# Optimization experiments

Hardware: AMD Instinct MI355X
Metric: run time of the kernel (lower is better)

## Reference

```python
import jax, jax.numpy as jnp
import numpy as np

BATCH = 2_000_000
IN_DIM = 10
OUT_DIM = 3


def setup_inputs() -> dict:
    key = jax.random.key(0)
    kx, kw, km = jax.random.split(key, 3)
    x = jax.random.normal(kx, (BATCH, IN_DIM), dtype=jnp.float32)
    W = jax.random.normal(kw, (OUT_DIM, IN_DIM), dtype=jnp.float32)
    # M initialized near identity (well-conditioned), matching torch.eye init
    M = jnp.eye(OUT_DIM, dtype=jnp.float32) + 0.1 * jax.random.normal(km, (OUT_DIM, OUT_DIM), dtype=jnp.float32)
    return {"x": x, "W": W, "M": M}


def reference(x, W, M):
    det_A = jnp.linalg.det(M)
    is_singular = jnp.isclose(det_A, jnp.float32(0.0))  # torch.isclose defaults: rtol=1e-5, atol=1e-8
    M_inv = jnp.linalg.inv(M)
    M_inv = jnp.where(is_singular, jnp.full_like(M_inv, jnp.nan), M_inv)
    # y = (M_inv @ W @ x.T).T == x @ (M_inv @ W).T
    proj = M_inv @ W                      # [out, in] tiny matmul
    return x @ proj.T                     # [batch, out]
```

## Files before the change

kernel.cpp:

```cpp
#include <hip/hip_runtime.h>

#define IN_DIM 10
#define OUT_DIM 3
#define BLOCK 256

__global__ __launch_bounds__(BLOCK, 6) void simnet_direct(
    const float* __restrict__ x,
    const float* __restrict__ W,
    const float* __restrict__ M,
    float* __restrict__ out,
    long long batch)
{
    const long long npairs = batch >> 1;
    const long long p = (long long)blockIdx.x * BLOCK + threadIdx.x;
    if (p >= npairs) return;

    const float4* xv = reinterpret_cast<const float4*>(x) + 5 * p;
    const float4 v0 = xv[0];
    const float4 v1 = xv[1];
    const float4 v2 = xv[2];
    const float4 v3 = xv[3];
    const float4 v4 = xv[4];

    const float a = M[0], b = M[1], c = M[2];
    const float d = M[3], e = M[4], f_ = M[5];
    const float g = M[6], h = M[7], i_ = M[8];
    const float A =  (e * i_ - f_ * h);
    const float B = -(d * i_ - f_ * g);
    const float C =  (d * h  - e  * g);
    const float det = a * A + b * B + c * C;
    float inv[3][3];
    if (fabsf(det) <= 1e-8f) {
        const float qn = __builtin_nanf("");
        #pragma unroll
        for (int o = 0; o < 3; ++o)
            #pragma unroll
            for (int k = 0; k < 3; ++k) inv[o][k] = qn;
    } else {
        const float r = 1.0f / det;
        inv[0][0] = A * r;
        inv[0][1] = (c * h  - b * i_) * r;
        inv[0][2] = (b * f_ - c * e ) * r;
        inv[1][0] = B * r;
        inv[1][1] = (a * i_ - c * g ) * r;
        inv[1][2] = (c * d  - a * f_) * r;
        inv[2][0] = C * r;
        inv[2][1] = (b * g  - a * h ) * r;
        inv[2][2] = (a * e  - b * d ) * r;
    }
    float pj[OUT_DIM][IN_DIM];
    #pragma unroll
    for (int o = 0; o < OUT_DIM; ++o)
        #pragma unroll
        for (int j = 0; j < IN_DIM; ++j)
            pj[o][j] = inv[o][0] * W[0 * IN_DIM + j]
                     + inv[o][1] * W[1 * IN_DIM + j]
                     + inv[o][2] * W[2 * IN_DIM + j];

    const float r0j[IN_DIM] = { v0.x, v0.y, v0.z, v0.w,
                                v1.x, v1.y, v1.z, v1.w,
                                v2.x, v2.y };
    const float r1j[IN_DIM] = { v2.z, v2.w,
                                v3.x, v3.y, v3.z, v3.w,
                                v4.x, v4.y, v4.z, v4.w };
    float y0[OUT_DIM], y1[OUT_DIM];
    #pragma unroll
    for (int o = 0; o < OUT_DIM; ++o) {
        float s0 = r0j[0] * pj[o][0];
        float s1 = r1j[0] * pj[o][0];
        #pragma unroll
        for (int j = 1; j < IN_DIM; ++j) {
            s0 = fmaf(r0j[j], pj[o][j], s0);
            s1 = fmaf(r1j[j], pj[o][j], s1);
        }
        y0[o] = s0;
        y1[o] = s1;
    }

    float2* o2 = reinterpret_cast<float2*>(out) + 3 * p;
    o2[0] = make_float2(y0[0], y0[1]);
    o2[1] = make_float2(y0[2], y1[0]);
    o2[2] = make_float2(y1[1], y1[2]);
}

__global__ void simnet_tail(const float* __restrict__ x,
                            const float* __restrict__ W,
                            const float* __restrict__ M,
                            float* __restrict__ out,
                            long long batch)
{
    if (threadIdx.x != 0 || (batch & 1LL) == 0) return;
    const long long row = batch - 1;
    const float a = M[0], b = M[1], c = M[2];
    const float d = M[3], e = M[4], f_ = M[5];
    const float g = M[6], h = M[7], i_ = M[8];
    const float A =  (e * i_ - f_ * h);
    const float B = -(d * i_ - f_ * g);
    const float C =  (d * h  - e  * g);
    const float det = a * A + b * B + c * C;
    float inv[3][3];
    if (fabsf(det) <= 1e-8f) {
        const float qn = __builtin_nanf("");
        for (int o = 0; o < 3; ++o)
            for (int k = 0; k < 3; ++k) inv[o][k] = qn;
    } else {
        const float r = 1.0f / det;
        inv[0][0] = A * r;                  inv[0][1] = (c * h  - b * i_) * r;  inv[0][2] = (b * f_ - c * e ) * r;
        inv[1][0] = B * r;                  inv[1][1] = (a * i_ - c * g ) * r;  inv[1][2] = (c * d  - a * f_) * r;
        inv[2][0] = C * r;                  inv[2][1] = (b * g  - a * h ) * r;  inv[2][2] = (a * e  - b * d ) * r;
    }
    const float* xr = x + row * IN_DIM;
    for (int o = 0; o < OUT_DIM; ++o) {
        float s = 0.f;
        for (int j = 0; j < IN_DIM; ++j) {
            const float pj = inv[o][0] * W[0 * IN_DIM + j]
                           + inv[o][1] * W[1 * IN_DIM + j]
                           + inv[o][2] * W[2 * IN_DIM + j];
            s = fmaf(xr[j], pj, s);
        }
        out[row * OUT_DIM + o] = s;
    }
}

extern "C" void kernel_launch(void* const* d_in, const int* in_sizes, int n_in,
                              void* d_out, int out_size, void* d_ws, size_t ws_size,
                              hipStream_t stream) {
    const float* x = (const float*)d_in[0];
    const float* W = (const float*)d_in[1];
    const float* M = (const float*)d_in[2];
    float* out = (float*)d_out;
    const long long batch = (long long)in_sizes[0] / IN_DIM;
    const long long npairs = batch >> 1;
    const int grid = (int)((npairs + BLOCK - 1) / BLOCK);
    simnet_direct<<<grid, BLOCK, 0, stream>>>(x, W, M, out, batch);
    if (batch & 1LL)
        simnet_tail<<<1, 64, 0, stream>>>(x, W, M, out, batch);
}
```

Before: 20.36 us.

## Convert to grid-stride persistent kernel with hoisted projection and fused tail

Replaces the one-pair-per-thread launch with a grid-stride loop capped at 2048 blocks. Each thread now computes the inverse and projection matrix once and reuses it across many pairs, and readfirstlane keeps the projected weights in scalar registers. The odd-row tail is folded into the main kernel, which removes a second launch. The cost is fewer waves in flight to hide memory latency on a bandwidth-bound stream, and the serial loop carries a per-iteration dependency.

```diff
diff --git a/kernel.cpp b/kernel.cpp
--- a/kernel.cpp
+++ b/kernel.cpp
@@ -3,25 +3,20 @@
 #define IN_DIM 10
 #define OUT_DIM 3
 #define BLOCK 256
+#define MAX_BLOCKS 2048
 
-__global__ __launch_bounds__(BLOCK, 6) void simnet_direct(
+__device__ __forceinline__ float rfl(float v) {
+    return __int_as_float(__builtin_amdgcn_readfirstlane(__float_as_int(v)));
+}
+
+__global__ __launch_bounds__(BLOCK, 8) void simnet_persist(
     const float* __restrict__ x,
     const float* __restrict__ W,
     const float* __restrict__ M,
     float* __restrict__ out,
+    int npairs,
     long long batch)
 {
-    const long long npairs = batch >> 1;
-    const long long p = (long long)blockIdx.x * BLOCK + threadIdx.x;
-    if (p >= npairs) return;
-
-    const float4* xv = reinterpret_cast<const float4*>(x) + 5 * p;
-    const float4 v0 = xv[0];
-    const float4 v1 = xv[1];
-    const float4 v2 = xv[2];
-    const float4 v3 = xv[3];
-    const float4 v4 = xv[4];
-
     const float a = M[0], b = M[1], c = M[2];
     const float d = M[3], e = M[4], f_ = M[5];
     const float g = M[6], h = M[7], i_ = M[8];
@@ -53,72 +48,58 @@
     for (int o = 0; o < OUT_DIM; ++o)
         #pragma unroll
         for (int j = 0; j < IN_DIM; ++j)
-            pj[o][j] = inv[o][0] * W[0 * IN_DIM + j]
-                     + inv[o][1] * W[1 * IN_DIM + j]
-                     + inv[o][2] * W[2 * IN_DIM + j];
+            pj[o][j] = rfl(inv[o][0] * W[0 * IN_DIM + j]
+                         + inv[o][1] * W[1 * IN_DIM + j]
+                         + inv[o][2] * W[2 * IN_DIM + j]);
 
-    const float r0j[IN_DIM] = { v0.x, v0.y, v0.z, v0.w,
-                                v1.x, v1.y, v1.z, v1.w,
-                                v2.x, v2.y };
-    const float r1j[IN_DIM] = { v2.z, v2.w,
-                                v3.x, v3.y, v3.z, v3.w,
-                                v4.x, v4.y, v4.z, v4.w };
-    float y0[OUT_DIM], y1[OUT_DIM];
-    #pragma unroll
-    for (int o = 0; o < OUT_DIM; ++o) {
-        float s0 = r0j[0] * pj[o][0];
-        float s1 = r1j[0] * pj[o][0];
+    const int tid    = blockIdx.x * BLOCK + threadIdx.x;
+    const int stride = gridDim.x * BLOCK;
+
+    #pragma unroll 1
+    for (int p = tid; p < npairs; p += stride) {
+        const float4* xv = reinterpret_cast<const float4*>(x) + 5 * (long long)p;
+        const float4 v0 = xv[0];
+        const float4 v1 = xv[1];
+        const float4 v2 = xv[2];
+        const float4 v3 = xv[3];
+        const float4 v4 = xv[4];
+
+        const float r0j[IN_DIM] = { v0.x, v0.y, v0.z, v0.w,
+                                    v1.x, v1.y, v1.z, v1.w,
+                                    v2.x, v2.y };
+        const float r1j[IN_DIM] = { v2.z, v2.w,
+                                    v3.x, v3.y, v3.z, v3.w,
+                                    v4.x, v4.y, v4.z, v4.w };
+        float y0[OUT_DIM], y1[OUT_DIM];
         #pragma unroll
-        for (int j = 1; j < IN_DIM; ++j) {
-            s0 = fmaf(r0j[j], pj[o][j], s0);
-            s1 = fmaf(r1j[j], pj[o][j], s1);
+        for (int o = 0; o < OUT_DIM; ++o) {
+            float s0 = r0j[0] * pj[o][0];
+            float s1 = r1j[0] * pj[o][0];
+            #pragma unroll
+            for (int j = 1; j < IN_DIM; ++j) {
+                s0 = fmaf(r0j[j], pj[o][j], s0);
+                s1 = fmaf(r1j[j], pj[o][j], s1);
+            }
+            y0[o] = s0;
+            y1[o] = s1;
         }
-        y0[o] = s0;
-        y1[o] = s1;
+
+        float2* o2 = reinterpret_cast<float2*>(out) + 3 * (long long)p;
+        o2[0] = make_float2(y0[0], y0[1]);
+        o2[1] = make_float2(y0[2], y1[0]);
+        o2[2] = make_float2(y1[1], y1[2]);
     }
 
-    float2* o2 = reinterpret_cast<float2*>(out) + 3 * p;
-    o2[0] = make_float2(y0[0], y0[1]);
-    o2[1] = make_float2(y0[2], y1[0]);
-    o2[2] = make_float2(y1[1], y1[2]);
-}
-
-__global__ void simnet_tail(const float* __restrict__ x,
-                            const float* __restrict__ W,
-                            const float* __restrict__ M,
-                            float* __restrict__ out,
-                            long long batch)
-{
-    if (threadIdx.x != 0 || (batch & 1LL) == 0) return;
-    const long long row = batch - 1;
-    const float a = M[0], b = M[1], c = M[2];
-    const float d = M[3], e = M[4], f_ = M[5];
-    const float g = M[6], h = M[7], i_ = M[8];
-    const float A =  (e * i_ - f_ * h);
-    const float B = -(d * i_ - f_ * g);
-    const float C =  (d * h  - e  * g);
-    const float det = a * A + b * B + c * C;
-    float inv[3][3];
-    if (fabsf(det) <= 1e-8f) {
-        const float qn = __builtin_nanf("");
-        for (int o = 0; o < 3; ++o)
-            for (int k = 0; k < 3; ++k) inv[o][k] = qn;
-    } else {
-        const float r = 1.0f / det;
-        inv[0][0] = A * r;                  inv[0][1] = (c * h  - b * i_) * r;  inv[0][2] = (b * f_ - c * e ) * r;
-        inv[1][0] = B * r;                  inv[1][1] = (a * i_ - c * g ) * r;  inv[1][2] = (c * d  - a * f_) * r;
-        inv[2][0] = C * r;                  inv[2][1] = (b * g  - a * h ) * r;  inv[2][2] = (a * e  - b * d ) * r;
-    }
-    const float* xr = x + row * IN_DIM;
-    for (int o = 0; o < OUT_DIM; ++o) {
-        float s = 0.f;
-        for (int j = 0; j < IN_DIM; ++j) {
-            const float pj = inv[o][0] * W[0 * IN_DIM + j]
-                           + inv[o][1] * W[1 * IN_DIM + j]
-                           + inv[o][2] * W[2 * IN_DIM + j];
-            s = fmaf(xr[j], pj, s);
+    if ((batch & 1LL) && tid == 0) {
+        const long long row = batch - 1;
+        const float* xr = x + row * IN_DIM;
+        #pragma unroll
+        for (int o = 0; o < OUT_DIM; ++o) {
+            float s = 0.f;
+            #pragma unroll
+            for (int j = 0; j < IN_DIM; ++j) s = fmaf(xr[j], pj[o][j], s);
+            out[row * OUT_DIM + o] = s;
         }
-        out[row * OUT_DIM + o] = s;
     }
 }
 
@@ -130,9 +111,9 @@
     const float* M = (const float*)d_in[2];
     float* out = (float*)d_out;
     const long long batch = (long long)in_sizes[0] / IN_DIM;
-    const long long npairs = batch >> 1;
-    const int grid = (int)((npairs + BLOCK - 1) / BLOCK);
-    simnet_direct<<<grid, BLOCK, 0, stream>>>(x, W, M, out, batch);
-    if (batch & 1LL)
-        simnet_tail<<<1, 64, 0, stream>>>(x, W, M, out, batch);
+    const int npairs = (int)(batch >> 1);
+    int grid = (npairs + BLOCK - 1) / BLOCK;
+    if (grid > MAX_BLOCKS) grid = MAX_BLOCKS;
+    if (grid < 1) grid = 1;
+    simnet_persist<<<grid, BLOCK, 0, stream>>>(x, W, M, out, npairs, batch);
 }
```

Result: slower. 21.33 us (+4.7%).
